# Kernel tuning notes

Measured on AMD Instinct MI355X. Metric: run time of the kernel, lower is better.

The kernel has to match this reference:

```python
import jax, jax.numpy as jnp
import numpy as np


def setup_inputs() -> dict:
    key = jax.random.key(0)
    ks = jax.random.split(key, 7)
    B, C, N, F = 4, 8, 2048, 64
    H, O = 64, 64
    s_in = 1.0 / np.sqrt(F)
    s_h = 1.0 / np.sqrt(H)
    return {
        "x": jax.random.normal(ks[0], (B, C, N, F), dtype=jnp.float32),
        "W1": jax.random.uniform(ks[1], (H, F), jnp.float32, -s_in, s_in),
        "b1": jax.random.uniform(ks[2], (H,), jnp.float32, -s_in, s_in),
        "W2": jax.random.uniform(ks[3], (H, F), jnp.float32, -s_in, s_in),
        "b2": jax.random.uniform(ks[4], (H,), jnp.float32, -s_in, s_in),
        "W3": jax.random.uniform(ks[5], (O, F), jnp.float32, -s_in, s_in),
        "b3": jax.random.uniform(ks[6], (O,), jnp.float32, -s_in, s_in),
    }


def reference(x, W1, b1, W2, b2, W3, b3):
    # e1, e2: [B,C,N,H]  (torch Linear: x @ W^T + b)
    e1 = jnp.einsum("bcnf,hf->bcnh", x, W1) + b1
    e2 = jnp.einsum("bcnf,hf->bcnh", x, W2) + b2
    # adjacency via ReLU(e1 @ e2^T): [B,C,N,N]
    adj = jax.nn.relu(jnp.einsum("bcnh,bcmh->bcnm", e1, e2))
    # propagate: [B,C,N,F]
    h = jnp.einsum("bcnm,bcmf->bcnf", adj, x)
    # output projection (linear3): [B,C,N,O]
    return jnp.einsum("bcnf,of->bcno", h, W3) + b3
```

## Files before the change

### kernel.cpp

```cpp
#include <hip/hip_runtime.h>
#include <hip/hip_bf16.h>

#define BCH 32
#define NN  2048
#define DD  64

typedef __attribute__((ext_vector_type(8)))  __bf16 bf16x8;
typedef __attribute__((ext_vector_type(4)))  __bf16 bf16x4;
typedef __attribute__((ext_vector_type(4)))  float  f32x4;
typedef __attribute__((ext_vector_type(16))) float  f32x16;
typedef __attribute__((ext_vector_type(2)))  int    i32x2;
typedef __attribute__((ext_vector_type(4)))  int    i32x4;
typedef __attribute__((ext_vector_type(2)))  unsigned int u32x2;

__device__ inline f32x4 mfma16(bf16x8 a, bf16x8 b, f32x4 c) {
    return __builtin_amdgcn_mfma_f32_16x16x32_bf16(a, b, c, 0, 0, 0);
}
__device__ inline f32x16 mfma32(bf16x8 a, bf16x8 b, f32x16 c) {
    return __builtin_amdgcn_mfma_f32_32x32x16_bf16(a, b, c, 0, 0, 0);
}
__device__ inline void plswap(int& a, int& b) {
    u32x2 r = __builtin_amdgcn_permlane32_swap((unsigned)a, (unsigned)b, false, false);
    a = (int)r[0];
    b = (int)r[1];
}

__global__ __launch_bounds__(256) void prep_kernel(
    const float* __restrict__ x,
    const float* __restrict__ W1, const float* __restrict__ b1,
    const float* __restrict__ W2, const float* __restrict__ b2,
    const float* __restrict__ W3,
    __bf16* __restrict__ e1f, __bf16* __restrict__ e2f, __bf16* __restrict__ vtf)
{
    const int t   = threadIdx.x;
    const int blk = blockIdx.x;
    const int bc  = blk >> 5, st = blk & 31;
    const long grow = (long)bc * NN + st * 64;
    const int w = t >> 6, l = t & 63, lg = l >> 4, li = l & 15;

    bf16x8 a[4][2];
    #pragma unroll
    for (int nb = 0; nb < 4; ++nb)
        #pragma unroll
        for (int kk = 0; kk < 2; ++kk) {
            const float* p = x + (grow + nb * 16 + li) * DD + kk * 32 + lg * 8;
            f32x4 v0 = *(const f32x4*)p, v1 = *(const f32x4*)(p + 4);
            #pragma unroll
            for (int j = 0; j < 4; ++j) {
                a[nb][kk][j]     = (__bf16)v0[j];
                a[nb][kk][4 + j] = (__bf16)v1[j];
            }
        }

    bf16x8 wf1[2], wf2[2], wf3[2];
    #pragma unroll
    for (int kk = 0; kk < 2; ++kk) {
        const float* p1 = W1 + (w * 16 + li) * DD + kk * 32 + lg * 8;
        const float* p2 = W2 + (w * 16 + li) * DD + kk * 32 + lg * 8;
        const float* p3 = W3 + (w * 16 + li) * DD + kk * 32 + lg * 8;
        f32x4 u0 = *(const f32x4*)p1, u1 = *(const f32x4*)(p1 + 4);
        f32x4 v0 = *(const f32x4*)p2, v1 = *(const f32x4*)(p2 + 4);
        f32x4 t0 = *(const f32x4*)p3, t1 = *(const f32x4*)(p3 + 4);
        #pragma unroll
        for (int j = 0; j < 4; ++j) {
            wf1[kk][j] = (__bf16)u0[j]; wf1[kk][4 + j] = (__bf16)u1[j];
            wf2[kk][j] = (__bf16)v0[j]; wf2[kk][4 + j] = (__bf16)v1[j];
            wf3[kk][j] = (__bf16)t0[j]; wf3[kk][4 + j] = (__bf16)t1[j];
        }
    }
    const f32x4 bq1 = *(const f32x4*)(b1 + w * 16 + lg * 4);
    const f32x4 bq2 = *(const f32x4*)(b2 + w * 16 + lg * 4);

    const size_t tbase = (size_t)(bc * 32 + st) * 4096;

    #pragma unroll
    for (int nb = 0; nb < 4; ++nb) {
        f32x4 acc1 = {0.f,0.f,0.f,0.f}, acc2 = {0.f,0.f,0.f,0.f}, acc3 = {0.f,0.f,0.f,0.f};
        #pragma unroll
        for (int kk = 0; kk < 2; ++kk) {
            acc1 = mfma16(wf1[kk], a[nb][kk], acc1);
            acc2 = mfma16(wf2[kk], a[nb][kk], acc2);
            acc3 = mfma16(a[nb][kk], wf3[kk], acc3);
        }
        bf16x4 q1, q2, q3;
        #pragma unroll
        for (int r = 0; r < 4; ++r) {
            q1[r] = (__bf16)(acc1[r] + bq1[r]);
            q2[r] = (__bf16)(acc2[r] + bq2[r]);
            q3[r] = (__bf16)acc3[r];
        }
        *(bf16x4*)&e1f[tbase + (w * 2 + (lg >> 1)) * 512 + (nb * 16 + li) * 8 + (lg & 1) * 4] = q1;
        *(bf16x4*)&e2f[tbase + (w * 2 + (lg >> 1)) * 512 + (nb * 16 + li) * 8 + (lg & 1) * 4] = q2;
        *(bf16x4*)&vtf[tbase + (nb * 2 + (lg >> 1)) * 512 + (w * 16 + li) * 8 + (lg & 1) * 4] = q3;
    }
}

__global__ __launch_bounds__(256, 3) void fused_kernel(
    const __bf16* __restrict__ e1f, const __bf16* __restrict__ e2f,
    const __bf16* __restrict__ vtf, const float* __restrict__ b3,
    float* __restrict__ out)
{
    __shared__ float scratch[4096];

    const int t   = threadIdx.x;
    const int bid = blockIdx.x;
    const int x8 = bid & 7, jj = bid >> 3;
    const int bc = x8 * 4 + (jj >> 5), nt = jj & 31;

    const int w = t >> 6, l = t & 63;
    const int wn = w & 1, wm = w >> 1;
    const int l31 = l & 31, hi5 = l >> 5;
    const int nbase = nt * 64 + wn * 32;

    const float bv0 = b3[l31], bv1 = b3[32 + l31];

    bf16x8 e1v[4];
    {
        const __bf16* p = e1f + ((size_t)bc * 32 + nt) * 4096 + hi5 * 512 + (wn * 32 + l31) * 8;
        #pragma unroll
        for (int kk = 0; kk < 4; ++kk)
            e1v[kk] = *(const bf16x8*)(p + kk * 1024);
    }

    f32x16 fz;
    #pragma unroll
    for (int i = 0; i < 16; ++i) fz[i] = 0.f;
    f32x16 haccE[2], haccO[2];
    #pragma unroll
    for (int fb = 0; fb < 2; ++fb)
        #pragma unroll
        for (int i = 0; i < 16; ++i) { haccE[fb][i] = 0.f; haccO[fb][i] = 0.f; }

    const __bf16* E2 = e2f + (size_t)bc * 131072 + hi5 * 512 + (wm * 32 + l31) * 8;
    const __bf16* VT = vtf + (size_t)bc * 131072 + (wm * 4 + hi5) * 512 + l31 * 8;

    auto loadEF = [&](int kt, bf16x8 (&ef)[4]) {
        const __bf16* p = E2 + (size_t)kt * 4096;
        #pragma unroll
        for (int kk = 0; kk < 4; ++kk)
            ef[kk] = *(const bf16x8*)(p + kk * 1024);
    };
    auto loadVF = [&](int kt, bf16x8 (&vf)[4]) {
        const __bf16* p = VT + (size_t)kt * 4096;
        #pragma unroll
        for (int kk2 = 0; kk2 < 2; ++kk2) {
            vf[kk2 * 2 + 0] = *(const bf16x8*)(p + kk2 * 1024);
            vf[kk2 * 2 + 1] = *(const bf16x8*)(p + kk2 * 1024 + 256);
        }
    };
    auto computeS = [&](bf16x8 (&ef)[4], f32x16& sT) {
        sT = mfma32(ef[0], e1v[0], fz);
        #pragma unroll
        for (int kk = 1; kk < 4; ++kk)
            sT = mfma32(ef[kk], e1v[kk], sT);
    };
    auto packQ = [&](const f32x16& sT, i32x2 (&Q)[4]) {
        #pragma unroll
        for (int g = 0; g < 4; ++g) {
            bf16x4 q0;
            #pragma unroll
            for (int r = 0; r < 4; ++r) {
                float v = sT[4 * g + r];
                q0[r] = (__bf16)(v > 0.f ? v : 0.f);
            }
            Q[g] = __builtin_bit_cast(i32x2, q0);
        }
    };
    auto doPV = [&](i32x2 (&Q)[4], bf16x8 (&vf)[4], f32x16 (&acc)[2]) {
        #pragma unroll
        for (int kk2 = 0; kk2 < 2; ++kk2) {
            int a0 = Q[2 * kk2][0],     a1 = Q[2 * kk2][1];
            int b0 = Q[2 * kk2 + 1][0], b1 = Q[2 * kk2 + 1][1];
            plswap(a0, b0);
            plswap(a1, b1);
            i32x4 pfi = { a0, a1, b0, b1 };
            bf16x8 pf = __builtin_bit_cast(bf16x8, pfi);
            acc[0] = mfma32(pf, vf[kk2 * 2 + 0], acc[0]);
            acc[1] = mfma32(pf, vf[kk2 * 2 + 1], acc[1]);
        }
    };

    bf16x8 efA[4], vfA[4], efB[4], vfB[4];
    i32x2 Qa[4], Qb[4];
    f32x16 sT;

    loadEF(0, efA); loadVF(0, vfA);
    for (int kt = 0; kt < 32; kt += 2) {
        loadEF(kt + 1, efB); loadVF(kt + 1, vfB);
        computeS(efA, sT);
        packQ(sT, Qa);
        doPV(Qa, vfA, haccE);
        if (kt + 2 < 32) { loadEF(kt + 2, efA); loadVF(kt + 2, vfA); }
        computeS(efB, sT);
        packQ(sT, Qb);
        doPV(Qb, vfB, haccO);
    }

    f32x16 hacc[2];
    #pragma unroll
    for (int fb = 0; fb < 2; ++fb)
        #pragma unroll
        for (int i = 0; i < 16; ++i) hacc[fb][i] = haccE[fb][i] + haccO[fb][i];

    if (wm == 1) {
        #pragma unroll
        for (int q = 0; q < 8; ++q) {
            f32x4 v;
            #pragma unroll
            for (int r = 0; r < 4; ++r) {
                const int idx = q * 4 + r;
                v[r] = hacc[idx >> 4][idx & 15];
            }
            *(f32x4*)&scratch[wn * 2048 + q * 256 + l * 4] = v;
        }
    }
    __syncthreads();
    if (wm == 0) {
        #pragma unroll
        for (int q = 0; q < 8; ++q) {
            f32x4 v = *(const f32x4*)&scratch[wn * 2048 + q * 256 + l * 4];
            #pragma unroll
            for (int r = 0; r < 4; ++r) {
                const int idx = q * 4 + r;
                hacc[idx >> 4][idx & 15] += v[r];
            }
        }
        const size_t ob = ((size_t)bc * NN + nbase) * DD;
        #pragma unroll
        for (int reg = 0; reg < 16; ++reg) {
            const int n = (reg & 3) + 8 * (reg >> 2) + 4 * hi5;
            out[ob + (size_t)n * DD + l31]      = hacc[0][reg] + bv0;
            out[ob + (size_t)n * DD + 32 + l31] = hacc[1][reg] + bv1;
        }
    }
}

extern "C" void kernel_launch(void* const* d_in, const int* in_sizes, int n_in,
                              void* d_out, int out_size, void* d_ws, size_t ws_size,
                              hipStream_t stream) {
    const float* x  = (const float*)d_in[0];
    const float* W1 = (const float*)d_in[1];
    const float* b1 = (const float*)d_in[2];
    const float* W2 = (const float*)d_in[3];
    const float* b2 = (const float*)d_in[4];
    const float* W3 = (const float*)d_in[5];
    const float* b3 = (const float*)d_in[6];
    float* out = (float*)d_out;

    __bf16* e1f = (__bf16*)d_ws;
    __bf16* e2f = e1f + (size_t)BCH * NN * DD;
    __bf16* vtf = e2f + (size_t)BCH * NN * DD;

    prep_kernel<<<dim3(1024), dim3(256), 0, stream>>>(x, W1, b1, W2, b2, W3, e1f, e2f, vtf);
    fused_kernel<<<dim3(1024), dim3(256), 0, stream>>>(e1f, e2f, vtf, b3, out);
}
```

Baseline: 67.91 us.

## Give each wave two 32-row query tiles so loaded K/V fragments feed both

```diff
diff --git a/kernel.cpp b/kernel.cpp
--- a/kernel.cpp
+++ b/kernel.cpp
@@ -95,7 +95,7 @@
     }
 }
 
-__global__ __launch_bounds__(256, 3) void fused_kernel(
+__global__ __launch_bounds__(128, 2) void fused_kernel(
     const __bf16* __restrict__ e1f, const __bf16* __restrict__ e2f,
     const __bf16* __restrict__ vtf, const float* __restrict__ b3,
     float* __restrict__ out)
@@ -107,29 +107,31 @@
     const int x8 = bid & 7, jj = bid >> 3;
     const int bc = x8 * 4 + (jj >> 5), nt = jj & 31;
 
-    const int w = t >> 6, l = t & 63;
-    const int wn = w & 1, wm = w >> 1;
+    const int wm = t >> 6, l = t & 63;
     const int l31 = l & 31, hi5 = l >> 5;
-    const int nbase = nt * 64 + wn * 32;
+    const int nbase = nt * 64;
 
     const float bv0 = b3[l31], bv1 = b3[32 + l31];
 
-    bf16x8 e1v[4];
-    {
-        const __bf16* p = e1f + ((size_t)bc * 32 + nt) * 4096 + hi5 * 512 + (wn * 32 + l31) * 8;
+    bf16x8 e1v[2][4];
+    #pragma unroll
+    for (int nb = 0; nb < 2; ++nb) {
+        const __bf16* p = e1f + ((size_t)bc * 32 + nt) * 4096 + hi5 * 512 + (nb * 32 + l31) * 8;
         #pragma unroll
         for (int kk = 0; kk < 4; ++kk)
-            e1v[kk] = *(const bf16x8*)(p + kk * 1024);
+            e1v[nb][kk] = *(const bf16x8*)(p + kk * 1024);
     }
 
     f32x16 fz;
     #pragma unroll
     for (int i = 0; i < 16; ++i) fz[i] = 0.f;
-    f32x16 haccE[2], haccO[2];
-    #pragma unroll
-    for (int fb = 0; fb < 2; ++fb)
-        #pragma unroll
-        for (int i = 0; i < 16; ++i) { haccE[fb][i] = 0.f; haccO[fb][i] = 0.f; }
+    f32x16 hacc[2][2];
+    #pragma unroll
+    for (int nb = 0; nb < 2; ++nb)
+        #pragma unroll
+        for (int fb = 0; fb < 2; ++fb)
+            #pragma unroll
+            for (int i = 0; i < 16; ++i) hacc[nb][fb][i] = 0.f;
 
     const __bf16* E2 = e2f + (size_t)bc * 131072 + hi5 * 512 + (wm * 32 + l31) * 8;
     const __bf16* VT = vtf + (size_t)bc * 131072 + (wm * 4 + hi5) * 512 + l31 * 8;
@@ -148,89 +150,95 @@
             vf[kk2 * 2 + 1] = *(const bf16x8*)(p + kk2 * 1024 + 256);
         }
     };
-    auto computeS = [&](bf16x8 (&ef)[4], f32x16& sT) {
-        sT = mfma32(ef[0], e1v[0], fz);
-        #pragma unroll
-        for (int kk = 1; kk < 4; ++kk)
-            sT = mfma32(ef[kk], e1v[kk], sT);
-    };
-    auto packQ = [&](const f32x16& sT, i32x2 (&Q)[4]) {
-        #pragma unroll
-        for (int g = 0; g < 4; ++g) {
-            bf16x4 q0;
-            #pragma unroll
-            for (int r = 0; r < 4; ++r) {
-                float v = sT[4 * g + r];
-                q0[r] = (__bf16)(v > 0.f ? v : 0.f);
-            }
-            Q[g] = __builtin_bit_cast(i32x2, q0);
-        }
-    };
-    auto doPV = [&](i32x2 (&Q)[4], bf16x8 (&vf)[4], f32x16 (&acc)[2]) {
-        #pragma unroll
-        for (int kk2 = 0; kk2 < 2; ++kk2) {
-            int a0 = Q[2 * kk2][0],     a1 = Q[2 * kk2][1];
-            int b0 = Q[2 * kk2 + 1][0], b1 = Q[2 * kk2 + 1][1];
-            plswap(a0, b0);
-            plswap(a1, b1);
-            i32x4 pfi = { a0, a1, b0, b1 };
-            bf16x8 pf = __builtin_bit_cast(bf16x8, pfi);
-            acc[0] = mfma32(pf, vf[kk2 * 2 + 0], acc[0]);
-            acc[1] = mfma32(pf, vf[kk2 * 2 + 1], acc[1]);
-        }
+    auto computeS = [&](bf16x8 (&ef)[4], f32x16 (&sT)[2]) {
+        sT[0] = mfma32(ef[0], e1v[0][0], fz);
+        sT[1] = mfma32(ef[0], e1v[1][0], fz);
+        #pragma unroll
+        for (int kk = 1; kk < 4; ++kk) {
+            sT[0] = mfma32(ef[kk], e1v[0][kk], sT[0]);
+            sT[1] = mfma32(ef[kk], e1v[1][kk], sT[1]);
+        }
+    };
+    auto packQ = [&](const f32x16 (&sT)[2], i32x2 (&Q)[2][4]) {
+        #pragma unroll
+        for (int nb = 0; nb < 2; ++nb)
+            #pragma unroll
+            for (int g = 0; g < 4; ++g) {
+                bf16x4 q0;
+                #pragma unroll
+                for (int r = 0; r < 4; ++r)
+                    q0[r] = (__bf16)fmaxf(sT[nb][4 * g + r], 0.f);
+                Q[nb][g] = __builtin_bit_cast(i32x2, q0);
+            }
+    };
+    auto doPV = [&](i32x2 (&Q)[2][4], bf16x8 (&vf)[4]) {
+        #pragma unroll
+        for (int kk2 = 0; kk2 < 2; ++kk2)
+            #pragma unroll
+            for (int nb = 0; nb < 2; ++nb) {
+                int a0 = Q[nb][2 * kk2][0],     a1 = Q[nb][2 * kk2][1];
+                int b0 = Q[nb][2 * kk2 + 1][0], b1 = Q[nb][2 * kk2 + 1][1];
+                plswap(a0, b0);
+                plswap(a1, b1);
+                i32x4 pfi = { a0, a1, b0, b1 };
+                bf16x8 pf = __builtin_bit_cast(bf16x8, pfi);
+                hacc[nb][0] = mfma32(pf, vf[kk2 * 2 + 0], hacc[nb][0]);
+                hacc[nb][1] = mfma32(pf, vf[kk2 * 2 + 1], hacc[nb][1]);
+            }
     };
 
     bf16x8 efA[4], vfA[4], efB[4], vfB[4];
-    i32x2 Qa[4], Qb[4];
-    f32x16 sT;
+    i32x2 Qa[2][4], Qb[2][4];
+    f32x16 sT[2];
 
     loadEF(0, efA); loadVF(0, vfA);
     for (int kt = 0; kt < 32; kt += 2) {
         loadEF(kt + 1, efB); loadVF(kt + 1, vfB);
         computeS(efA, sT);
         packQ(sT, Qa);
-        doPV(Qa, vfA, haccE);
+        doPV(Qa, vfA);
         if (kt + 2 < 32) { loadEF(kt + 2, efA); loadVF(kt + 2, vfA); }
         computeS(efB, sT);
         packQ(sT, Qb);
-        doPV(Qb, vfB, haccO);
-    }
-
-    f32x16 hacc[2];
-    #pragma unroll
-    for (int fb = 0; fb < 2; ++fb)
-        #pragma unroll
-        for (int i = 0; i < 16; ++i) hacc[fb][i] = haccE[fb][i] + haccO[fb][i];
+        doPV(Qb, vfB);
+    }
 
     if (wm == 1) {
         #pragma unroll
-        for (int q = 0; q < 8; ++q) {
-            f32x4 v;
-            #pragma unroll
-            for (int r = 0; r < 4; ++r) {
-                const int idx = q * 4 + r;
-                v[r] = hacc[idx >> 4][idx & 15];
-            }
-            *(f32x4*)&scratch[wn * 2048 + q * 256 + l * 4] = v;
-        }
+        for (int nb = 0; nb < 2; ++nb)
+            #pragma unroll
+            for (int q = 0; q < 8; ++q) {
+                f32x4 v;
+                #pragma unroll
+                for (int r = 0; r < 4; ++r) {
+                    const int idx = q * 4 + r;
+                    v[r] = hacc[nb][idx >> 4][idx & 15];
+                }
+                *(f32x4*)&scratch[nb * 2048 + q * 256 + l * 4] = v;
+            }
     }
     __syncthreads();
     if (wm == 0) {
         #pragma unroll
-        for (int q = 0; q < 8; ++q) {
-            f32x4 v = *(const f32x4*)&scratch[wn * 2048 + q * 256 + l * 4];
-            #pragma unroll
-            for (int r = 0; r < 4; ++r) {
-                const int idx = q * 4 + r;
-                hacc[idx >> 4][idx & 15] += v[r];
-            }
-        }
-        const size_t ob = ((size_t)bc * NN + nbase) * DD;
-        #pragma unroll
-        for (int reg = 0; reg < 16; ++reg) {
-            const int n = (reg & 3) + 8 * (reg >> 2) + 4 * hi5;
-            out[ob + (size_t)n * DD + l31]      = hacc[0][reg] + bv0;
-            out[ob + (size_t)n * DD + 32 + l31] = hacc[1][reg] + bv1;
+        for (int nb = 0; nb < 2; ++nb)
+            #pragma unroll
+            for (int q = 0; q < 8; ++q) {
+                f32x4 v = *(const f32x4*)&scratch[nb * 2048 + q * 256 + l * 4];
+                #pragma unroll
+                for (int r = 0; r < 4; ++r) {
+                    const int idx = q * 4 + r;
+                    hacc[nb][idx >> 4][idx & 15] += v[r];
+                }
+            }
+        #pragma unroll
+        for (int nb = 0; nb < 2; ++nb) {
+            const size_t ob = ((size_t)bc * NN + nbase + nb * 32) * DD;
+            #pragma unroll
+            for (int reg = 0; reg < 16; ++reg) {
+                const int n = (reg & 3) + 8 * (reg >> 2) + 4 * hi5;
+                out[ob + (size_t)n * DD + l31]      = hacc[nb][0][reg] + bv0;
+                out[ob + (size_t)n * DD + 32 + l31] = hacc[nb][1][reg] + bv1;
+            }
         }
     }
 }
@@ -252,5 +260,5 @@
     __bf16* vtf = e2f + (size_t)BCH * NN * DD;
 
     prep_kernel<<<dim3(1024), dim3(256), 0, stream>>>(x, W1, b1, W2, b2, W3, e1f, e2f, vtf);
-    fused_kernel<<<dim3(1024), dim3(256), 0, stream>>>(e1f, e2f, vtf, b3, out);
-}
+    fused_kernel<<<dim3(1024), dim3(128), 0, stream>>>(e1f, e2f, vtf, b3, out);
+}
```

New measurement: 59.86 us. 1.13x faster.
